# Kernel optimization log

Hardware: AMD Instinct MI355X
Metric: run time of the kernel (lower is better)

Reference implementation:

```python
import jax, jax.numpy as jnp
import numpy as np

NUM_USERS = 400000  # matches fill_max of indexes in input_specs
K = 10              # top_k from init_kwargs
NEG_INF = -1000000000.0


def setup_inputs() -> dict:
    key = jax.random.key(0)
    k1, k2, k3 = jax.random.split(key, 3)
    N = 8000000
    predictions = jax.random.normal(k1, (N,), dtype=jnp.float32)
    targets = jax.random.uniform(k2, (N,), dtype=jnp.float32)
    indexes = jax.random.randint(k3, (N,), 0, NUM_USERS, dtype=jnp.int64)
    return {"predictions": predictions, "targets": targets, "indexes": indexes}


def reference(predictions, targets, indexes):
    # Faithful to the torch source, which does `counts_per_user[u] = 1` (not +=1):
    # column 0 holds each user's FIRST occurrence, column 1 holds the LAST
    # occurrence (subsequent scatters to pos 1 overwrite), everything else is
    # padding (-1e9 preds / 0 targets). Padding columns beyond k provably don't
    # affect topk/dcg/idcg, so we use a static width of K.
    n = predictions.shape[0]
    pos = jnp.arange(n, dtype=jnp.int32)
    seg = indexes.astype(jnp.int32)
    first = jax.ops.segment_min(pos, seg, num_segments=NUM_USERS)
    last = jax.ops.segment_max(pos, seg, num_segments=NUM_USERS)
    counts = jax.ops.segment_sum(jnp.ones_like(pos), seg, num_segments=NUM_USERS)
    has2 = counts >= 2  # pos 1 is only ever written on a second occurrence

    p0 = predictions[first]
    t0 = targets[first]
    p1 = jnp.where(has2, predictions[last], NEG_INF)
    t1 = jnp.where(has2, targets[last], 0.0)

    pred_padded = jnp.full((NUM_USERS, K), NEG_INF, dtype=predictions.dtype)
    pred_padded = pred_padded.at[:, 0].set(p0).at[:, 1].set(p1)
    target_padded = jnp.zeros((NUM_USERS, K), dtype=targets.dtype)
    target_padded = target_padded.at[:, 0].set(t0).at[:, 1].set(t1)

    _, topk_idx = jax.lax.top_k(pred_padded, K)
    topk_targets = jnp.take_along_axis(target_padded, topk_idx, axis=1)
    discounts = jnp.log2(jnp.arange(2, K + 2, dtype=jnp.float32))
    dcg = (topk_targets / discounts).sum(axis=1)
    ideal = -jnp.sort(-target_padded, axis=1)  # descending sort
    idcg = (ideal[:, :K] / discounts).sum(axis=1)
    return (dcg / idcg).mean()
```

## Files before the change

### kernel.cpp

```cpp
#include <hip/hip_runtime.h>
#include <climits>

static constexpr int NUSERS = 400000;
static constexpr float NEG_INF_F = -1000000000.0f;
static constexpr float INV_LOG2_3 = 0.6309297535714575f;

static constexpr int USLICE_LOG = 11;
static constexpr int USLICE = 1 << USLICE_LOG;
static constexpr int S = 196;
static constexpr int CHUNK = 4096;
static constexpr int CPG = 255;
static constexpr int GSPAN = CHUNK * CPG;
static constexpr int G = 8;
static constexpr int CAP = 6144;


__global__ void k_init_part(int* __restrict__ cursor, float* __restrict__ acc) {
    int t = blockIdx.x * blockDim.x + threadIdx.x;
    if (t < G * S) cursor[t] = 0;
    if (t == G * S) acc[0] = 0.0f;
}

__global__ __launch_bounds__(256, 6) void k_scatter(const int* __restrict__ idx, int n,
                                                    unsigned* __restrict__ records,
                                                    int* __restrict__ cursor) {
    __shared__ int cnt[S];
    __shared__ int base_l[S + 1];
    __shared__ int base_g[S];
    __shared__ unsigned stage[CHUNK];
    __shared__ unsigned char stage_s[CHUNK];

    const int t = threadIdx.x;
    const int g = blockIdx.x / CPG;
    const int gbase = g * GSPAN;
    const int q0 = blockIdx.x * (CHUNK / 4);
    const int nq = n >> 2;
    const int4* idx4 = reinterpret_cast<const int4*>(idx);

    int4 v[4];
    int rnk[16];
#pragma unroll
    for (int k = 0; k < 4; ++k) {
        int q = q0 + k * 256 + t;
        v[k] = (q < nq) ? idx4[q] : make_int4(-1, -1, -1, -1);
    }

    if (t < S) cnt[t] = 0;
    __syncthreads();

#pragma unroll
    for (int k = 0; k < 4; ++k) {
        int us[4] = {v[k].x, v[k].y, v[k].z, v[k].w};
#pragma unroll
        for (int e = 0; e < 4; ++e)
            rnk[k * 4 + e] = (us[e] >= 0) ? atomicAdd(&cnt[us[e] >> USLICE_LOG], 1) : 0;
    }
    __syncthreads();

    if (t < 64) {
        int v0 = cnt[t];
        int v1 = (64 + t < S) ? cnt[64 + t] : 0;
        int v2 = (128 + t < S) ? cnt[128 + t] : 0;
        int v3 = (192 + t < S) ? cnt[192 + t] : 0;
        int a = v0, b = v1, c = v2, d = v3;
#pragma unroll
        for (int dd = 1; dd < 64; dd <<= 1) { int y = __shfl_up(a, dd, 64); if (t >= dd) a += y; }
        int ta = __shfl(a, 63, 64);
#pragma unroll
        for (int dd = 1; dd < 64; dd <<= 1) { int y = __shfl_up(b, dd, 64); if (t >= dd) b += y; }
        int tb = __shfl(b, 63, 64);
#pragma unroll
        for (int dd = 1; dd < 64; dd <<= 1) { int y = __shfl_up(c, dd, 64); if (t >= dd) c += y; }
        int tc = __shfl(c, 63, 64);
#pragma unroll
        for (int dd = 1; dd < 64; dd <<= 1) { int y = __shfl_up(d, dd, 64); if (t >= dd) d += y; }
        int td = __shfl(d, 63, 64);
        b += ta; c += ta + tb; d += ta + tb + tc;
        base_l[t] = a - v0;
        if (64 + t < S)  base_l[64 + t]  = b - v1;
        if (128 + t < S) base_l[128 + t] = c - v2;
        if (192 + t < S) base_l[192 + t] = d - v3;
        if (t == 0) base_l[S] = ta + tb + tc + td;
    }
    if (t < S) base_g[t] = atomicAdd(&cursor[g * S + t], cnt[t]);
    __syncthreads();

#pragma unroll
    for (int k = 0; k < 4; ++k) {
        int q = q0 + k * 256 + t;
        int us[4] = {v[k].x, v[k].y, v[k].z, v[k].w};
#pragma unroll
        for (int e = 0; e < 4; ++e) {
            int u = us[e];
            if (u >= 0) {
                int s = u >> USLICE_LOG;
                int pos = base_l[s] + rnk[k * 4 + e];
                unsigned iloc = (unsigned)(q * 4 + e - gbase);
                stage[pos] = ((unsigned)(u & (USLICE - 1)) << 20) | iloc;
                stage_s[pos] = (unsigned char)s;
            }
        }
    }
    __syncthreads();

    int total = base_l[S];
    for (int r = t; r < total; r += 256) {
        unsigned rec = stage[r];
        int s = stage_s[r];
        int pos = base_g[s] + (r - base_l[s]);
        if (pos < CAP)
            records[(size_t)(g * S + s) * CAP + pos] = rec;
    }
}

__global__ __launch_bounds__(1024, 4) void k_reduce_ndcg(
        const unsigned* __restrict__ records, const int* __restrict__ cursor,
        const float* __restrict__ pred, const float* __restrict__ tgt,
        int n, float* __restrict__ acc) {
    __shared__ int tabf[USLICE];
    __shared__ int tabl[USLICE];
    const int s = blockIdx.x;
    const int t = threadIdx.x;

    for (int u = t; u < USLICE; u += 1024) { tabf[u] = INT_MAX; tabl[u] = -1; }
    __syncthreads();

    for (int g = 0; g < G; ++g) {
        int cnt = min(cursor[g * S + s], CAP);
        const uint4* base4 = reinterpret_cast<const uint4*>(records + (size_t)(g * S + s) * CAP);
        const int gb = g * GSPAN;
        for (int p4 = t; p4 * 4 < cnt; p4 += 1024) {
            uint4 vv = base4[p4];
            int p = p4 * 4;
            unsigned rr[4] = {vv.x, vv.y, vv.z, vv.w};
#pragma unroll
            for (int e = 0; e < 4; ++e) {
                if (p + e < cnt) {
                    int loc = rr[e] >> 20;
                    int i = (int)(rr[e] & 0xFFFFFu) + gb;
                    atomicMin(&tabf[loc], i);
                    atomicMax(&tabl[loc], i);
                }
            }
        }
    }
    __syncthreads();

    float v = 0.0f;
    for (int uu = t; uu < USLICE; uu += 1024) {
        int u = s * USLICE + uu;
        if (u < NUSERS) {
            int f = tabf[uu];
            int l = tabl[uu];
            f = min(f, n - 1);
            float p0 = pred[f];
            float t0 = tgt[f];
            bool has2 = l > f;
            float p1 = has2 ? pred[l] : NEG_INF_F;
            float t1 = has2 ? tgt[l] : 0.0f;
            float dcg  = (p0 >= p1) ? fmaf(t1, INV_LOG2_3, t0) : fmaf(t0, INV_LOG2_3, t1);
            float idcg = fmaf(fminf(t0, t1), INV_LOG2_3, fmaxf(t0, t1));
            v += dcg / idcg;
        }
    }
    for (int off = 32; off > 0; off >>= 1) v += __shfl_down(v, off, 64);
    __shared__ float wsum[16];
    int lane = t & 63, wid = t >> 6;
    if (lane == 0) wsum[wid] = v;
    __syncthreads();
    if (t == 0) {
        float ss = 0.0f;
#pragma unroll
        for (int w = 0; w < 16; ++w) ss += wsum[w];
        atomicAdd(acc, ss);
    }
}

__global__ void k_final(const float* __restrict__ acc, float* __restrict__ out) {
    out[0] = acc[0] * (1.0f / (float)NUSERS);
}


__global__ void k_init_fb(int* __restrict__ first, int* __restrict__ last,
                          float* __restrict__ acc) {
    int i = blockIdx.x * blockDim.x + threadIdx.x;
    if (i < NUSERS) { first[i] = INT_MAX; last[i] = -1; }
    if (i == 0) acc[0] = 0.0f;
}

__global__ void k_minmax_fb(const int* __restrict__ idx, int* __restrict__ first,
                            int* __restrict__ last, int n) {
    int base = (blockIdx.x * blockDim.x + threadIdx.x) * 4;
    if (base + 3 < n) {
        int4 u4 = *reinterpret_cast<const int4*>(idx + base);
        int us[4] = {u4.x, u4.y, u4.z, u4.w};
#pragma unroll
        for (int j = 0; j < 4; ++j) {
            int u = us[j], i = base + j;
            if (i < first[u]) atomicMin(&first[u], i);
            if (i > last[u])  atomicMax(&last[u], i);
        }
    } else {
        for (int i = base; i < n; ++i) {
            int u = idx[i];
            if (i < first[u]) atomicMin(&first[u], i);
            if (i > last[u])  atomicMax(&last[u], i);
        }
    }
}

__global__ void k_ndcg_fb(const float* __restrict__ pred, const float* __restrict__ tgt,
                          const int* __restrict__ first, const int* __restrict__ last,
                          int n, float* __restrict__ acc) {
    int u = blockIdx.x * blockDim.x + threadIdx.x;
    float v = 0.0f;
    if (u < NUSERS) {
        int f = min(first[u], n - 1);
        int l = last[u];
        float p0 = pred[f], t0 = tgt[f];
        bool has2 = l > f;
        float p1 = has2 ? pred[l] : NEG_INF_F;
        float t1 = has2 ? tgt[l] : 0.0f;
        float dcg  = (p0 >= p1) ? fmaf(t1, INV_LOG2_3, t0) : fmaf(t0, INV_LOG2_3, t1);
        float idcg = fmaf(fminf(t0, t1), INV_LOG2_3, fmaxf(t0, t1));
        v = dcg / idcg;
    }
    for (int off = 32; off > 0; off >>= 1) v += __shfl_down(v, off, 64);
    __shared__ float wsum[4];
    int lane = threadIdx.x & 63, wid = threadIdx.x >> 6;
    if (lane == 0) wsum[wid] = v;
    __syncthreads();
    if (threadIdx.x == 0) atomicAdd(acc, wsum[0] + wsum[1] + wsum[2] + wsum[3]);
}


extern "C" void kernel_launch(void* const* d_in, const int* in_sizes, int n_in,
                              void* d_out, int out_size, void* d_ws, size_t ws_size,
                              hipStream_t stream) {
    const float* pred = (const float*)d_in[0];
    const float* tgt  = (const float*)d_in[1];
    const int*   idx  = (const int*)d_in[2];
    const int n = in_sizes[0];
    float* out = (float*)d_out;

    const size_t recs_bytes = (size_t)G * S * CAP * sizeof(unsigned);
    const size_t need = recs_bytes + 16384 + 64;

    if (ws_size >= need && n <= G * GSPAN && (n & 3) == 0) {
        unsigned* records = (unsigned*)d_ws;
        int* cursor = (int*)((char*)d_ws + recs_bytes);
        float* acc = (float*)((char*)d_ws + recs_bytes + 16384);

        k_init_part<<<(G * S + 256) / 256, 256, 0, stream>>>(cursor, acc);

        int nblocks = (n + CHUNK - 1) / CHUNK;
        k_scatter<<<nblocks, 256, 0, stream>>>(idx, n, records, cursor);

        k_reduce_ndcg<<<S, 1024, 0, stream>>>(records, cursor, pred, tgt, n, acc);

        k_final<<<1, 1, 0, stream>>>(acc, out);
    } else {
        int* first = (int*)d_ws;
        int* last  = first + NUSERS;
        float* acc = (float*)(last + NUSERS);

        k_init_fb<<<(NUSERS + 255) / 256, 256, 0, stream>>>(first, last, acc);
        int nq4 = (n + 3) / 4;
        k_minmax_fb<<<(nq4 + 255) / 256, 256, 0, stream>>>(idx, first, last, n);
        k_ndcg_fb<<<(NUSERS + 255) / 256, 256, 0, stream>>>(pred, tgt, first, last, n, acc);
        k_final<<<1, 1, 0, stream>>>(acc, out);
    }
}
```

Before: 157.1 us.

## Repartition users into 256 slices and pack slice id into staging word

Changes the user partition from 196 power-of-two slices of 2048 users to 256 slices of 1563 users. The reduce kernel, which runs one block per slice, now gets one block for each of the MI355X's 256 CUs instead of leaving some idle. The scatter kernel drops its separate byte array of slice ids and packs slice, local user and in-chunk position into one 32-bit staging word, then decodes it when writing to global memory. It also lowers the per-bucket capacity and raises the occupancy hint to 8. The cost is an integer division by a non-power-of-two constant and a tighter overflow margin per bucket.

```diff
diff --git a/kernel.cpp b/kernel.cpp
--- a/kernel.cpp
+++ b/kernel.cpp
@@ -5,14 +5,13 @@
 static constexpr float NEG_INF_F = -1000000000.0f;
 static constexpr float INV_LOG2_3 = 0.6309297535714575f;
 
-static constexpr int USLICE_LOG = 11;
-static constexpr int USLICE = 1 << USLICE_LOG;
-static constexpr int S = 196;
+static constexpr int USLICE = 1563;
+static constexpr int S = 256;
 static constexpr int CHUNK = 4096;
 static constexpr int CPG = 255;
 static constexpr int GSPAN = CHUNK * CPG;
 static constexpr int G = 8;
-static constexpr int CAP = 6144;
+static constexpr int CAP = 4608;
 
 
 __global__ void k_init_part(int* __restrict__ cursor, float* __restrict__ acc) {
@@ -21,18 +20,17 @@
     if (t == G * S) acc[0] = 0.0f;
 }
 
-__global__ __launch_bounds__(256, 6) void k_scatter(const int* __restrict__ idx, int n,
+__global__ __launch_bounds__(256, 8) void k_scatter(const int* __restrict__ idx, int n,
                                                     unsigned* __restrict__ records,
                                                     int* __restrict__ cursor) {
     __shared__ int cnt[S];
     __shared__ int base_l[S + 1];
     __shared__ int base_g[S];
     __shared__ unsigned stage[CHUNK];
-    __shared__ unsigned char stage_s[CHUNK];
 
     const int t = threadIdx.x;
     const int g = blockIdx.x / CPG;
-    const int gbase = g * GSPAN;
+    const int cbase = blockIdx.x * CHUNK - g * GSPAN;
     const int q0 = blockIdx.x * (CHUNK / 4);
     const int nq = n >> 2;
     const int4* idx4 = reinterpret_cast<const int4*>(idx);
@@ -53,15 +51,15 @@
         int us[4] = {v[k].x, v[k].y, v[k].z, v[k].w};
 #pragma unroll
         for (int e = 0; e < 4; ++e)
-            rnk[k * 4 + e] = (us[e] >= 0) ? atomicAdd(&cnt[us[e] >> USLICE_LOG], 1) : 0;
+            rnk[k * 4 + e] = (us[e] >= 0) ? atomicAdd(&cnt[us[e] / USLICE], 1) : 0;
     }
     __syncthreads();
 
     if (t < 64) {
         int v0 = cnt[t];
-        int v1 = (64 + t < S) ? cnt[64 + t] : 0;
-        int v2 = (128 + t < S) ? cnt[128 + t] : 0;
-        int v3 = (192 + t < S) ? cnt[192 + t] : 0;
+        int v1 = cnt[64 + t];
+        int v2 = cnt[128 + t];
+        int v3 = cnt[192 + t];
         int a = v0, b = v1, c = v2, d = v3;
 #pragma unroll
         for (int dd = 1; dd < 64; dd <<= 1) { int y = __shfl_up(a, dd, 64); if (t >= dd) a += y; }
@@ -77,9 +75,9 @@
         int td = __shfl(d, 63, 64);
         b += ta; c += ta + tb; d += ta + tb + tc;
         base_l[t] = a - v0;
-        if (64 + t < S)  base_l[64 + t]  = b - v1;
-        if (128 + t < S) base_l[128 + t] = c - v2;
-        if (192 + t < S) base_l[192 + t] = d - v3;
+        base_l[64 + t] = b - v1;
+        base_l[128 + t] = c - v2;
+        base_l[192 + t] = d - v3;
         if (t == 0) base_l[S] = ta + tb + tc + td;
     }
     if (t < S) base_g[t] = atomicAdd(&cursor[g * S + t], cnt[t]);
@@ -87,17 +85,16 @@
 
 #pragma unroll
     for (int k = 0; k < 4; ++k) {
-        int q = q0 + k * 256 + t;
         int us[4] = {v[k].x, v[k].y, v[k].z, v[k].w};
 #pragma unroll
         for (int e = 0; e < 4; ++e) {
             int u = us[e];
             if (u >= 0) {
-                int s = u >> USLICE_LOG;
+                int s = u / USLICE;
+                int loc = u - s * USLICE;
                 int pos = base_l[s] + rnk[k * 4 + e];
-                unsigned iloc = (unsigned)(q * 4 + e - gbase);
-                stage[pos] = ((unsigned)(u & (USLICE - 1)) << 20) | iloc;
-                stage_s[pos] = (unsigned char)s;
+                unsigned pic = (unsigned)((k * 256 + t) * 4 + e);
+                stage[pos] = ((unsigned)s << 23) | ((unsigned)loc << 12) | pic;
             }
         }
     }
@@ -105,11 +102,13 @@
 
     int total = base_l[S];
     for (int r = t; r < total; r += 256) {
-        unsigned rec = stage[r];
-        int s = stage_s[r];
+        unsigned tmp = stage[r];
+        int s = tmp >> 23;
+        unsigned loc = (tmp >> 12) & 0x7FFu;
+        unsigned iloc = (unsigned)cbase + (tmp & 0xFFFu);
         int pos = base_g[s] + (r - base_l[s]);
         if (pos < CAP)
-            records[(size_t)(g * S + s) * CAP + pos] = rec;
+            records[(size_t)(g * S + s) * CAP + pos] = (loc << 20) | iloc;
     }
 }
 
```

Result: faster. 150.9 us (-4.0%).
